# Optimization experiments

Hardware: AMD Instinct MI355X
Metric: run time of the kernel (lower is better)

## Reference

```python
import jax, jax.numpy as jnp
import numpy as np

DIM_X = 256
DIM_E = 256
SCALE = (DIM_X + DIM_E) ** -0.5


def setup_inputs() -> dict:
    key = jax.random.key(0)
    k1, k2, k3, k4 = jax.random.split(key, 4)
    b, n = 8, 2048
    d = DIM_X + DIM_E
    x = jax.random.normal(k1, (b, n, DIM_X), dtype=jnp.float32)
    e = jax.random.normal(k2, (n, DIM_E), dtype=jnp.float32)
    # nn.Linear(d, d, bias=False) weights, torch layout (out, in): y = x @ W.T
    Wq = jax.random.normal(k3, (d, d), dtype=jnp.float32) * 0.02
    Wk = jax.random.normal(k4, (d, d), dtype=jnp.float32) * 0.02
    return {"x": x, "e": e, "Wq": Wq, "Wk": Wk}


def reference(x, e, Wq, Wk):
    b, n, t = x.shape
    # e repeated across batch, concatenated with x along feature dim
    e_b = jnp.broadcast_to(e[None], (b, n, e.shape[-1]))
    x_e = jnp.concatenate([x, e_b], axis=-1)            # (b, n, dX+dE)
    queries = x_e @ Wq.T                                 # (b, n, d)
    keys = x_e @ Wk.T                                    # (b, n, d)
    # raw bilinear scores, no softmax; dropout=0 (eval) is identity
    attn = jnp.einsum('bnd,bmd->bnm', queries, keys) * SCALE
    out = jnp.einsum('bnm,bmt->bnt', attn, x)            # v = x
    return out
```

## Files before the change

kernel.cpp:

```cpp
#include <hip/hip_runtime.h>
#include <hip/hip_bf16.h>

#define DIM_X 256
#define DIM_E 256
#define DD    512
#define NB    8
#define NN    2048
#define SCALE 0.044194173824159216f

typedef __attribute__((ext_vector_type(8))) __bf16 bf16x8;
typedef __attribute__((ext_vector_type(4))) float  f32x4;
using bf16 = __hip_bfloat16;

__device__ __forceinline__ unsigned short f2bf(float f) {
  union { __hip_bfloat16 h; unsigned short u; } c;
  c.h = __float2bfloat16(f);
  return c.u;
}

__device__ __forceinline__ void async_lds16(const void* g, void* l) {
  using u32_as3 = __attribute__((address_space(3))) unsigned int;
  using u32_as1 = const __attribute__((address_space(1))) unsigned int;
  __builtin_amdgcn_global_load_lds(
      reinterpret_cast<u32_as1*>(reinterpret_cast<unsigned long long>(g)),
      reinterpret_cast<u32_as3*>(static_cast<unsigned int>(
          reinterpret_cast<unsigned long long>(l))),
      16, 0, 0);
}

__global__ __launch_bounds__(256, 4) void pack_k(
    const float* __restrict__ x, const float* __restrict__ e,
    const float* __restrict__ Wq, const float* __restrict__ Wk, bf16* xb,
    bf16* VT, bf16* eb, bf16* ET, bf16* WqT, bf16* WkT) {
  __shared__ float tile[32][33];
  const int tid  = threadIdx.x;
  const int lrow = tid >> 3;
  const int lc4  = (tid & 7) * 4;
  const int j    = blockIdx.x;
  const float* src; int ld;
  bf16 *dS = nullptr, *dT; int ldS = 0, ldT;
  if (j < 4096) {
    int b = j & 7;
    int slot = j >> 3;
    int r = slot >> 3, c = slot & 7;
    src = x + ((long)b * NN + r * 32) * DIM_X + c * 32; ld = DIM_X;
    dS = xb + ((long)b * NN + r * 32) * DIM_X + c * 32; ldS = DIM_X;
    dT = VT + ((long)b * DIM_X + c * 32) * NN + r * 32; ldT = NN;
  } else if (j < 4608) {
    int i = j - 4096, r = i >> 3, c = i & 7;
    src = e + ((long)r * 32) * DIM_E + c * 32; ld = DIM_E;
    dS = eb + ((long)r * 32) * DIM_E + c * 32; ldS = DIM_E;
    dT = ET + ((long)c * 32) * NN + r * 32; ldT = NN;
  } else if (j < 4864) {
    int i = j - 4608, r = i >> 4, c = i & 15;
    src = Wq + ((long)r * 32) * DD + c * 32; ld = DD;
    dT = WqT + ((long)c * 32) * DD + r * 32; ldT = DD;
  } else {
    int i = j - 4864, r = i >> 4, c = i & 15;
    src = Wk + ((long)r * 32) * DD + c * 32; ld = DD;
    dT = WkT + ((long)c * 32) * DD + r * 32; ldT = DD;
  }
  float4 v = *(const float4*)(src + (long)lrow * ld + lc4);
  if (dS) {
    ushort4 o;
    o.x = f2bf(v.x); o.y = f2bf(v.y); o.z = f2bf(v.z); o.w = f2bf(v.w);
    *(ushort4*)((unsigned short*)dS + (long)lrow * ldS + lc4) = o;
  }
  tile[lrow][lc4 + 0] = v.x; tile[lrow][lc4 + 1] = v.y;
  tile[lrow][lc4 + 2] = v.z; tile[lrow][lc4 + 3] = v.w;
  __syncthreads();
  {
    ushort4 o;
    o.x = f2bf(tile[lc4 + 0][lrow]);
    o.y = f2bf(tile[lc4 + 1][lrow]);
    o.z = f2bf(tile[lc4 + 2][lrow]);
    o.w = f2bf(tile[lc4 + 3][lrow]);
    *(ushort4*)((unsigned short*)dT + (long)lrow * ldT + lc4) = o;
  }
}

template <int BM, int BN, int BKt, bool OUT_BF16, int ASPLIT, int BSPLIT>
__device__ void gemm_tile(const bf16* __restrict__ A0,
                          const bf16* __restrict__ A1,
                          const bf16* __restrict__ B0,
                          const bf16* __restrict__ B1, void* __restrict__ Cv,
                          int K, int lda, int ldb, int ldc, float alpha,
                          char* smem) {
  constexpr int CPT  = BKt / 8;
  constexpr int KS   = BKt / 32;
  constexpr int WTM  = BM / 2, WTN = BN / 2;
  constexpr int IM   = WTM / 16, IN = WTN / 16;
  constexpr int CA   = BM * CPT, CB = BN * CPT;
  constexpr int BUFB = (BM + BN) * BKt * 2;

  const int tid  = threadIdx.x;
  const int lane = tid & 63;
  const int wave = tid >> 6;
  const int lm   = lane & 15;
  const int quad = lane >> 4;
  const int wm   = (wave >> 1) * WTM;
  const int wn   = (wave & 1) * WTN;

  auto stage = [&](int t, int buf) {
    const int k0 = t * BKt;
    const bf16* Ak = A0; int ka = k0;
    if (ASPLIT > 0 && k0 >= ASPLIT) { Ak = A1; ka = k0 - ASPLIT; }
    const bf16* Bk = B0; int kb = k0;
    if (BSPLIT > 0 && k0 >= BSPLIT) { Bk = B1; kb = k0 - BSPLIT; }
    bf16* sA = (bf16*)(smem + (size_t)buf * BUFB);
    bf16* sB = sA + BM * BKt;
#pragma unroll
    for (int c = tid; c < CA; c += 256) {
      int row = c / CPT;
      int cb  = (c % CPT) ^ (row % CPT);
      async_lds16(Ak + (long)row * lda + ka + cb * 8, sA + (size_t)c * 8);
    }
#pragma unroll
    for (int c = tid; c < CB; c += 256) {
      int row = c / CPT;
      int cb  = (c % CPT) ^ (row % CPT);
      async_lds16(Bk + (long)row * ldb + kb + cb * 8, sB + (size_t)c * 8);
    }
  };

  f32x4 acc[IM][IN];
#pragma unroll
  for (int i = 0; i < IM; i++)
#pragma unroll
    for (int j = 0; j < IN; j++) acc[i][j] = (f32x4){0.f, 0.f, 0.f, 0.f};

  const int nt = K / BKt;
  stage(0, 0);
  __syncthreads();
  int cur = 0;
  for (int t = 0; t < nt; ++t) {
    if (t + 1 < nt) stage(t + 1, cur ^ 1);
    const bf16* sA = (const bf16*)(smem + (size_t)cur * BUFB);
    const bf16* sB = sA + BM * BKt;
    bf16x8 af[KS][IM], bfr[KS][IN];
#pragma unroll
    for (int s = 0; s < KS; s++) {
#pragma unroll
      for (int i = 0; i < IM; i++) {
        int r = wm + i * 16 + lm;
        af[s][i] = *(const bf16x8*)&sA[r * BKt +
                                       (((s * 4 + quad) ^ (r % CPT)) * 8)];
      }
#pragma unroll
      for (int j = 0; j < IN; j++) {
        int r = wn + j * 16 + lm;
        bfr[s][j] = *(const bf16x8*)&sB[r * BKt +
                                        (((s * 4 + quad) ^ (r % CPT)) * 8)];
      }
    }
#pragma unroll
    for (int s = 0; s < KS; s++)
#pragma unroll
      for (int i = 0; i < IM; i++)
#pragma unroll
        for (int j = 0; j < IN; j++)
          acc[i][j] = __builtin_amdgcn_mfma_f32_16x16x32_bf16(
              af[s][i], bfr[s][j], acc[i][j], 0, 0, 0);
    __syncthreads();
    cur ^= 1;
  }

  const int baseRow = wm + quad * 4;
  const int baseCol = wn + lm;
  if (OUT_BF16) {
    bf16* Cb = (bf16*)Cv;
#pragma unroll
    for (int i = 0; i < IM; i++)
#pragma unroll
      for (int r = 0; r < 4; r++) {
        int row = baseRow + i * 16 + r;
#pragma unroll
        for (int j = 0; j < IN; j++)
          Cb[(long)row * ldc + baseCol + j * 16] =
              __float2bfloat16(acc[i][j][r] * alpha);
      }
  } else {
    float* Cf = (float*)Cv;
#pragma unroll
    for (int i = 0; i < IM; i++)
#pragma unroll
      for (int r = 0; r < 4; r++) {
        int row = baseRow + i * 16 + r;
#pragma unroll
        for (int j = 0; j < IN; j++)
          Cf[(long)row * ldc + baseCol + j * 16] = acc[i][j][r] * alpha;
      }
  }
}

__global__ __launch_bounds__(256, 2) void phase1_k(
    const bf16* VT, const bf16* ET, const bf16* WqT, const bf16* WkT,
    bf16* M1, bf16* M2, bf16* W2T) {
  __shared__ __align__(16) char smem[49152];
  const int bx = blockIdx.x;
  if (bx < 256) {
    const int b   = bx & 7;
    const int idx = bx >> 3;
    const int kh  = idx & 1;
    const int mt  = (idx >> 1) & 1;
    const int nt  = idx >> 2;
    const bf16* A = VT + (long)b * DIM_X * NN + (long)mt * 128 * NN +
                    kh * 1024;
    const bf16* B = (nt < 4)
        ? VT + (long)b * DIM_X * NN + (long)nt * 64 * NN + kh * 1024
        : ET + (long)(nt - 4) * 64 * NN + kh * 1024;
    bf16* C = (kh ? M2 : M1) + (long)b * DIM_X * DD + (long)mt * 128 * DD +
              nt * 64;
    gemm_tile<128, 64, 64, true, 0, 0>(A, nullptr, B, nullptr, C, 1024, NN,
                                       NN, DD, 1.0f, smem);
  } else {
    const int i = bx - 256;
    int r2 = i >> 3, c2 = i & 7;
    gemm_tile<64, 64, 64, true, 0, 0>(
        WqT + (long)r2 * 64 * DD, nullptr, WkT + (long)c2 * 64 * DD, nullptr,
        W2T + (long)r2 * 64 * DD + c2 * 64, DD, DD, DD, DD, 1.0f, smem);
  }
}

__global__ __launch_bounds__(256, 3) void phase2_k(const bf16* M1,
                                                   const bf16* M2,
                                                   const bf16* W2T, bf16* R) {
  __shared__ __align__(16) char smem[49152];
  const int bx = blockIdx.x;
  const int b = bx & 7, r = (bx >> 3) & 7, c = bx >> 6;
  const bf16* a0 = M1 + (long)b * DIM_X * DD + (long)r * 32 * DD;
  const bf16* a1 = M2 + (long)b * DIM_X * DD + (long)r * 32 * DD;
  const bf16* w  = W2T + (long)c * 64 * DD;
  gemm_tile<32, 64, 128, true, 512, 512>(
      a0, a1, w, w, R + (long)b * DIM_X * DD + (long)r * 32 * DD + c * 64,
      1024, DD, DD, DD, SCALE, smem);
}

__global__ __launch_bounds__(256, 2) void phase3_k(const bf16* xb,
                                                   const bf16* eb,
                                                   const bf16* R, float* out) {
  __shared__ __align__(16) char smem[65536];
  const int bx = blockIdx.x;
  const int b = bx & 7, m = (bx >> 3) & 15, n = (bx >> 7) & 1;
  gemm_tile<128, 128, 64, false, 256, 0>(
      xb + (long)b * NN * DIM_X + (long)m * 128 * DIM_X,
      eb + (long)m * 128 * DIM_E,
      R + (long)b * DIM_X * DD + (long)n * 128 * DD, nullptr,
      out + (long)b * NN * DIM_X + (long)m * 128 * DIM_X + n * 128, DD,
      DIM_X, DD, DIM_X, 1.0f, smem);
}


extern "C" void kernel_launch(void* const* d_in, const int* in_sizes, int n_in,
                              void* d_out, int out_size, void* d_ws,
                              size_t ws_size, hipStream_t stream) {
  const float* x  = (const float*)d_in[0];
  const float* e  = (const float*)d_in[1];
  const float* Wq = (const float*)d_in[2];
  const float* Wk = (const float*)d_in[3];
  float* out = (float*)d_out;

  char* ws = (char*)d_ws;
  size_t off = 0;
  auto alloc = [&](size_t bytes) {
    void* p = ws + off;
    off += (bytes + 255) & ~(size_t)255;
    return p;
  };

  bf16* xb  = (bf16*)alloc((size_t)NB * NN * DIM_X * 2);
  bf16* VT  = (bf16*)alloc((size_t)NB * DIM_X * NN * 2);
  bf16* eb  = (bf16*)alloc((size_t)NN * DIM_E * 2);
  bf16* ET  = (bf16*)alloc((size_t)DIM_E * NN * 2);
  bf16* WqT = (bf16*)alloc((size_t)DD * DD * 2);
  bf16* WkT = (bf16*)alloc((size_t)DD * DD * 2);
  bf16* W2T = (bf16*)alloc((size_t)DD * DD * 2);
  bf16* M1  = (bf16*)alloc((size_t)NB * DIM_X * DD * 2);
  bf16* M2  = (bf16*)alloc((size_t)NB * DIM_X * DD * 2);
  bf16* R   = (bf16*)alloc((size_t)NB * DIM_X * DD * 2);

  pack_k<<<5120, 256, 0, stream>>>(x, e, Wq, Wk, xb, VT, eb, ET, WqT, WkT);
  phase1_k<<<320, 256, 0, stream>>>(VT, ET, WqT, WkT, M1, M2, W2T);
  phase2_k<<<512, 256, 0, stream>>>(M1, M2, W2T, R);
  phase3_k<<<256, 256, 0, stream>>>(xb, eb, R, out);
}
```

Baseline: 105.3 us.

## Reassociate bilinear attention chain into three kernels with fused W2 product

Changes the association order of the chain. W2R = Wk^T·Wq is computed directly from fp32 weights inside the pack kernel. Then x·W2R, e·W2R and the Gram-like M = x^T·[x|e] are computed in one middle kernel, and a final K=1024 GEMM produces the output. This drops one launch and the separate phase2 step. In exchange it materialises a large Px intermediate (b×n×512 bf16) and does more FLOPs in the middle stage, while no longer splitting the K dimension of M.

```diff
diff --git a/kernel.cpp b/kernel.cpp
--- a/kernel.cpp
+++ b/kernel.cpp
@@ -26,57 +26,6 @@
       reinterpret_cast<u32_as3*>(static_cast<unsigned int>(
           reinterpret_cast<unsigned long long>(l))),
       16, 0, 0);
-}
-
-__global__ __launch_bounds__(256, 4) void pack_k(
-    const float* __restrict__ x, const float* __restrict__ e,
-    const float* __restrict__ Wq, const float* __restrict__ Wk, bf16* xb,
-    bf16* VT, bf16* eb, bf16* ET, bf16* WqT, bf16* WkT) {
-  __shared__ float tile[32][33];
-  const int tid  = threadIdx.x;
-  const int lrow = tid >> 3;
-  const int lc4  = (tid & 7) * 4;
-  const int j    = blockIdx.x;
-  const float* src; int ld;
-  bf16 *dS = nullptr, *dT; int ldS = 0, ldT;
-  if (j < 4096) {
-    int b = j & 7;
-    int slot = j >> 3;
-    int r = slot >> 3, c = slot & 7;
-    src = x + ((long)b * NN + r * 32) * DIM_X + c * 32; ld = DIM_X;
-    dS = xb + ((long)b * NN + r * 32) * DIM_X + c * 32; ldS = DIM_X;
-    dT = VT + ((long)b * DIM_X + c * 32) * NN + r * 32; ldT = NN;
-  } else if (j < 4608) {
-    int i = j - 4096, r = i >> 3, c = i & 7;
-    src = e + ((long)r * 32) * DIM_E + c * 32; ld = DIM_E;
-    dS = eb + ((long)r * 32) * DIM_E + c * 32; ldS = DIM_E;
-    dT = ET + ((long)c * 32) * NN + r * 32; ldT = NN;
-  } else if (j < 4864) {
-    int i = j - 4608, r = i >> 4, c = i & 15;
-    src = Wq + ((long)r * 32) * DD + c * 32; ld = DD;
-    dT = WqT + ((long)c * 32) * DD + r * 32; ldT = DD;
-  } else {
-    int i = j - 4864, r = i >> 4, c = i & 15;
-    src = Wk + ((long)r * 32) * DD + c * 32; ld = DD;
-    dT = WkT + ((long)c * 32) * DD + r * 32; ldT = DD;
-  }
-  float4 v = *(const float4*)(src + (long)lrow * ld + lc4);
-  if (dS) {
-    ushort4 o;
-    o.x = f2bf(v.x); o.y = f2bf(v.y); o.z = f2bf(v.z); o.w = f2bf(v.w);
-    *(ushort4*)((unsigned short*)dS + (long)lrow * ldS + lc4) = o;
-  }
-  tile[lrow][lc4 + 0] = v.x; tile[lrow][lc4 + 1] = v.y;
-  tile[lrow][lc4 + 2] = v.z; tile[lrow][lc4 + 3] = v.w;
-  __syncthreads();
-  {
-    ushort4 o;
-    o.x = f2bf(tile[lc4 + 0][lrow]);
-    o.y = f2bf(tile[lc4 + 1][lrow]);
-    o.z = f2bf(tile[lc4 + 2][lrow]);
-    o.w = f2bf(tile[lc4 + 3][lrow]);
-    *(ushort4*)((unsigned short*)dT + (long)lrow * ldT + lc4) = o;
-  }
 }
 
 template <int BM, int BN, int BKt, bool OUT_BF16, int ASPLIT, int BSPLIT>
@@ -193,61 +142,211 @@
   }
 }
 
-__global__ __launch_bounds__(256, 2) void phase1_k(
-    const bf16* VT, const bf16* ET, const bf16* WqT, const bf16* WkT,
-    bf16* M1, bf16* M2, bf16* W2T) {
+__device__ void w2r_tile(const float* __restrict__ Wk,
+                         const float* __restrict__ Wq,
+                         bf16* __restrict__ W2R, int j0, int i0, char* smem) {
+  float (*scr)[65] = reinterpret_cast<float (*)[65]>(smem);
+  unsigned short* Ab = (unsigned short*)(smem + 16640);
+  unsigned short* Bb = Ab + 64 * 72;
+  const int tid  = threadIdx.x;
+  const int lane = tid & 63;
+  const int wv   = tid >> 6;
+  const int lm   = lane & 15;
+  const int quad = lane >> 4;
+  const int wm   = (wv >> 1) * 32;
+  const int wn   = (wv & 1) * 32;
+  const int lrow = tid >> 2;
+  const int lc   = (tid & 3) * 16;
+  const int sj   = tid & 63;
+  const int sd0  = (tid >> 6) * 16;
+
+  f32x4 acc[2][2];
+#pragma unroll
+  for (int i = 0; i < 2; i++)
+#pragma unroll
+    for (int j = 0; j < 2; j++) acc[i][j] = (f32x4){0.f, 0.f, 0.f, 0.f};
+
+  for (int dc = 0; dc < DD; dc += 64) {
+    {
+      const float* s0 = Wk + (long)(dc + lrow) * DD + j0 + lc;
+      float4 v0 = *(const float4*)(s0 + 0);
+      float4 v1 = *(const float4*)(s0 + 4);
+      float4 v2 = *(const float4*)(s0 + 8);
+      float4 v3 = *(const float4*)(s0 + 12);
+      *(float4*)&scr[lrow][lc + 0]  = v0;
+      *(float4*)&scr[lrow][lc + 4]  = v1;
+      *(float4*)&scr[lrow][lc + 8]  = v2;
+      *(float4*)&scr[lrow][lc + 12] = v3;
+    }
+    __syncthreads();
+#pragma unroll
+    for (int g = 0; g < 4; g++) {
+      ushort4 o;
+      o.x = f2bf(scr[sd0 + g * 4 + 0][sj]);
+      o.y = f2bf(scr[sd0 + g * 4 + 1][sj]);
+      o.z = f2bf(scr[sd0 + g * 4 + 2][sj]);
+      o.w = f2bf(scr[sd0 + g * 4 + 3][sj]);
+      *(ushort4*)&Ab[sj * 72 + sd0 + g * 4] = o;
+    }
+    __syncthreads();
+    {
+      const float* s0 = Wq + (long)(dc + lrow) * DD + i0 + lc;
+      float4 v0 = *(const float4*)(s0 + 0);
+      float4 v1 = *(const float4*)(s0 + 4);
+      float4 v2 = *(const float4*)(s0 + 8);
+      float4 v3 = *(const float4*)(s0 + 12);
+      *(float4*)&scr[lrow][lc + 0]  = v0;
+      *(float4*)&scr[lrow][lc + 4]  = v1;
+      *(float4*)&scr[lrow][lc + 8]  = v2;
+      *(float4*)&scr[lrow][lc + 12] = v3;
+    }
+    __syncthreads();
+#pragma unroll
+    for (int g = 0; g < 4; g++) {
+      ushort4 o;
+      o.x = f2bf(scr[sd0 + g * 4 + 0][sj]);
+      o.y = f2bf(scr[sd0 + g * 4 + 1][sj]);
+      o.z = f2bf(scr[sd0 + g * 4 + 2][sj]);
+      o.w = f2bf(scr[sd0 + g * 4 + 3][sj]);
+      *(ushort4*)&Bb[sj * 72 + sd0 + g * 4] = o;
+    }
+    __syncthreads();
+#pragma unroll
+    for (int s = 0; s < 2; s++) {
+      bf16x8 af[2], bf_[2];
+#pragma unroll
+      for (int i = 0; i < 2; i++)
+        af[i] = *(const bf16x8*)&Ab[(wm + i * 16 + lm) * 72 + s * 32 +
+                                    quad * 8];
+#pragma unroll
+      for (int j = 0; j < 2; j++)
+        bf_[j] = *(const bf16x8*)&Bb[(wn + j * 16 + lm) * 72 + s * 32 +
+                                     quad * 8];
+#pragma unroll
+      for (int i = 0; i < 2; i++)
+#pragma unroll
+        for (int j = 0; j < 2; j++)
+          acc[i][j] = __builtin_amdgcn_mfma_f32_16x16x32_bf16(
+              af[i], bf_[j], acc[i][j], 0, 0, 0);
+    }
+    __syncthreads();
+  }
+  const int baseRow = wm + quad * 4;
+  const int baseCol = wn + lm;
+#pragma unroll
+  for (int i = 0; i < 2; i++)
+#pragma unroll
+    for (int r = 0; r < 4; r++)
+#pragma unroll
+      for (int j = 0; j < 2; j++)
+        W2R[(long)(j0 + baseRow + i * 16 + r) * DD + i0 + baseCol + j * 16] =
+            __float2bfloat16(acc[i][j][r]);
+}
+
+__global__ __launch_bounds__(256, 4) void pack2_k(
+    const float* __restrict__ x, const float* __restrict__ e,
+    const float* __restrict__ Wq, const float* __restrict__ Wk, bf16* xb,
+    bf16* VT, bf16* eb, bf16* ET, bf16* W2R) {
+  __shared__ __align__(16) char smem[35072];
+  const int j = blockIdx.x;
+  if (j >= 4608) {
+    const int i = j - 4608;
+    w2r_tile(Wk, Wq, W2R, (i >> 3) * 64, (i & 7) * 64, smem);
+    return;
+  }
+  float (*tile)[33] = reinterpret_cast<float (*)[33]>(smem);
+  const int tid  = threadIdx.x;
+  const int lrow = tid >> 3;
+  const int lc4  = (tid & 7) * 4;
+  const float* src; int ld;
+  bf16 *dS, *dT; int ldS, ldT;
+  if (j < 4096) {
+    int b = j & 7;
+    int slot = j >> 3;
+    int r = slot >> 3, c = slot & 7;
+    src = x + ((long)b * NN + r * 32) * DIM_X + c * 32; ld = DIM_X;
+    dS = xb + ((long)b * NN + r * 32) * DIM_X + c * 32; ldS = DIM_X;
+    dT = VT + ((long)b * DIM_X + c * 32) * NN + r * 32; ldT = NN;
+  } else {
+    int i = j - 4096, r = i >> 3, c = i & 7;
+    src = e + ((long)r * 32) * DIM_E + c * 32; ld = DIM_E;
+    dS = eb + ((long)r * 32) * DIM_E + c * 32; ldS = DIM_E;
+    dT = ET + ((long)c * 32) * NN + r * 32; ldT = NN;
+  }
+  float4 v = *(const float4*)(src + (long)lrow * ld + lc4);
+  {
+    ushort4 o;
+    o.x = f2bf(v.x); o.y = f2bf(v.y); o.z = f2bf(v.z); o.w = f2bf(v.w);
+    *(ushort4*)((unsigned short*)dS + (long)lrow * ldS + lc4) = o;
+  }
+  tile[lrow][lc4 + 0] = v.x; tile[lrow][lc4 + 1] = v.y;
+  tile[lrow][lc4 + 2] = v.z; tile[lrow][lc4 + 3] = v.w;
+  __syncthreads();
+  {
+    ushort4 o;
+    o.x = f2bf(tile[lc4 + 0][lrow]);
+    o.y = f2bf(tile[lc4 + 1][lrow]);
+    o.z = f2bf(tile[lc4 + 2][lrow]);
+    o.w = f2bf(tile[lc4 + 3][lrow]);
+    *(ushort4*)((unsigned short*)dT + (long)lrow * ldT + lc4) = o;
+  }
+}
+
+__global__ __launch_bounds__(256, 3) void mid_k(
+    const bf16* VT, const bf16* ET, const bf16* xb, const bf16* eb,
+    const bf16* W2R, bf16* M, bf16* Px, bf16* E2) {
   __shared__ __align__(16) char smem[49152];
   const int bx = blockIdx.x;
   if (bx < 256) {
-    const int b   = bx & 7;
+    const int b  = bx & 7;
     const int idx = bx >> 3;
-    const int kh  = idx & 1;
-    const int mt  = (idx >> 1) & 1;
-    const int nt  = idx >> 2;
-    const bf16* A = VT + (long)b * DIM_X * NN + (long)mt * 128 * NN +
-                    kh * 1024;
-    const bf16* B = (nt < 4)
-        ? VT + (long)b * DIM_X * NN + (long)nt * 64 * NN + kh * 1024
-        : ET + (long)(nt - 4) * 64 * NN + kh * 1024;
-    bf16* C = (kh ? M2 : M1) + (long)b * DIM_X * DD + (long)mt * 128 * DD +
-              nt * 64;
-    gemm_tile<128, 64, 64, true, 0, 0>(A, nullptr, B, nullptr, C, 1024, NN,
-                                       NN, DD, 1.0f, smem);
+    const int mt = idx & 3;
+    const int nt = idx >> 2;
+    const bf16* A = VT + (long)b * DIM_X * NN + (long)mt * 64 * NN;
+    const bf16* B = (nt < 4) ? VT + (long)b * DIM_X * NN + (long)nt * 64 * NN
+                             : ET + (long)(nt - 4) * 64 * NN;
+    gemm_tile<64, 64, 64, true, 0, 0>(
+        A, nullptr, B, nullptr,
+        M + (long)b * DIM_X * DD + (long)mt * 64 * DD + nt * 64, NN, NN, NN,
+        DD, 1.0f, smem);
+  } else if (bx < 1280) {
+    const int i  = bx - 256;
+    const int b  = i & 7;
+    const int idx = i >> 3;
+    const int nt = idx & 15;
+    const int ct = idx >> 4;
+    gemm_tile<128, 64, 64, true, 0, 0>(
+        xb + (long)b * NN * DIM_X + (long)nt * 128 * DIM_X, nullptr,
+        W2R + (long)ct * 64 * DD, nullptr,
+        Px + (long)b * NN * DD + (long)nt * 128 * DD + ct * 64, DIM_X, DIM_X,
+        DD, DD, 1.0f, smem);
   } else {
-    const int i = bx - 256;
-    int r2 = i >> 3, c2 = i & 7;
-    gemm_tile<64, 64, 64, true, 0, 0>(
-        WqT + (long)r2 * 64 * DD, nullptr, WkT + (long)c2 * 64 * DD, nullptr,
-        W2T + (long)r2 * 64 * DD + c2 * 64, DD, DD, DD, DD, 1.0f, smem);
-  }
-}
-
-__global__ __launch_bounds__(256, 3) void phase2_k(const bf16* M1,
-                                                   const bf16* M2,
-                                                   const bf16* W2T, bf16* R) {
-  __shared__ __align__(16) char smem[49152];
-  const int bx = blockIdx.x;
-  const int b = bx & 7, r = (bx >> 3) & 7, c = bx >> 6;
-  const bf16* a0 = M1 + (long)b * DIM_X * DD + (long)r * 32 * DD;
-  const bf16* a1 = M2 + (long)b * DIM_X * DD + (long)r * 32 * DD;
-  const bf16* w  = W2T + (long)c * 64 * DD;
-  gemm_tile<32, 64, 128, true, 512, 512>(
-      a0, a1, w, w, R + (long)b * DIM_X * DD + (long)r * 32 * DD + c * 64,
-      1024, DD, DD, DD, SCALE, smem);
-}
-
-__global__ __launch_bounds__(256, 2) void phase3_k(const bf16* xb,
-                                                   const bf16* eb,
-                                                   const bf16* R, float* out) {
+    const int i  = bx - 1280;
+    const int nt = i & 15;
+    const int ct = i >> 4;
+    gemm_tile<128, 64, 64, true, 0, 0>(
+        eb + (long)nt * 128 * DIM_E, nullptr,
+        W2R + DIM_X + (long)ct * 64 * DD, nullptr,
+        E2 + (long)nt * 128 * DD + ct * 64, DIM_E, DIM_E, DD, DD, 1.0f,
+        smem);
+  }
+}
+
+__global__ __launch_bounds__(256, 2) void out_k(const bf16* Px,
+                                                const bf16* E2, const bf16* M,
+                                                float* out) {
   __shared__ __align__(16) char smem[65536];
   const int bx = blockIdx.x;
-  const int b = bx & 7, m = (bx >> 3) & 15, n = (bx >> 7) & 1;
-  gemm_tile<128, 128, 64, false, 256, 0>(
-      xb + (long)b * NN * DIM_X + (long)m * 128 * DIM_X,
-      eb + (long)m * 128 * DIM_E,
-      R + (long)b * DIM_X * DD + (long)n * 128 * DD, nullptr,
-      out + (long)b * NN * DIM_X + (long)m * 128 * DIM_X + n * 128, DD,
-      DIM_X, DD, DIM_X, 1.0f, smem);
+  const int b  = bx & 7;
+  const int idx = bx >> 3;
+  const int m  = idx & 15;
+  const int n  = idx >> 4;
+  const bf16* Mb = M + (long)b * DIM_X * DD + (long)n * 128 * DD;
+  gemm_tile<128, 128, 64, false, 512, 512>(
+      Px + (long)b * NN * DD + (long)m * 128 * DD, E2 + (long)m * 128 * DD,
+      Mb, Mb,
+      out + (long)b * NN * DIM_X + (long)m * 128 * DIM_X + n * 128, 1024, DD,
+      DD, DIM_X, SCALE, smem);
 }
 
 
@@ -272,15 +371,12 @@
   bf16* VT  = (bf16*)alloc((size_t)NB * DIM_X * NN * 2);
   bf16* eb  = (bf16*)alloc((size_t)NN * DIM_E * 2);
   bf16* ET  = (bf16*)alloc((size_t)DIM_E * NN * 2);
-  bf16* WqT = (bf16*)alloc((size_t)DD * DD * 2);
-  bf16* WkT = (bf16*)alloc((size_t)DD * DD * 2);
-  bf16* W2T = (bf16*)alloc((size_t)DD * DD * 2);
-  bf16* M1  = (bf16*)alloc((size_t)NB * DIM_X * DD * 2);
-  bf16* M2  = (bf16*)alloc((size_t)NB * DIM_X * DD * 2);
-  bf16* R   = (bf16*)alloc((size_t)NB * DIM_X * DD * 2);
-
-  pack_k<<<5120, 256, 0, stream>>>(x, e, Wq, Wk, xb, VT, eb, ET, WqT, WkT);
-  phase1_k<<<320, 256, 0, stream>>>(VT, ET, WqT, WkT, M1, M2, W2T);
-  phase2_k<<<512, 256, 0, stream>>>(M1, M2, W2T, R);
-  phase3_k<<<256, 256, 0, stream>>>(xb, eb, R, out);
-}
+  bf16* W2R = (bf16*)alloc((size_t)DD * DD * 2);
+  bf16* M   = (bf16*)alloc((size_t)NB * DIM_X * DD * 2);
+  bf16* Px  = (bf16*)alloc((size_t)NB * NN * DD * 2);
+  bf16* E2  = (bf16*)alloc((size_t)NN * DD * 2);
+
+  pack2_k<<<4672, 256, 0, stream>>>(x, e, Wq, Wk, xb, VT, eb, ET, W2R);
+  mid_k<<<1408, 256, 0, stream>>>(VT, ET, xb, eb, W2R, M, Px, E2);
+  out_k<<<256, 256, 0, stream>>>(Px, E2, M, out);
+}
```

Result: slower. 131.3 us (+24.7%).
